# Performance work log

Measured on AMD Instinct MI355X. Metric: run time of the kernel, lower is better.

The kernel has to match this reference:

```python
import jax, jax.numpy as jnp
import numpy as np


def _conv2d(x, w, stride, padding):
    # x: NCHW, w: OIHW
    return jax.lax.conv_general_dilated(
        x, w, window_strides=(stride, stride),
        padding=((padding, padding), (padding, padding)),
        dimension_numbers=('NCHW', 'OIHW', 'NCHW'))


def setup_inputs() -> dict:
    key = jax.random.key(0)
    k1, k2 = jax.random.split(key)
    B, C_in, H, Wd = 8, 64, 256, 256
    C_out, ksz = 64, 3
    x = jax.random.normal(k1, (B, C_in, H, Wd), dtype=jnp.float32)
    W = jax.random.normal(k2, (C_out, C_in, ksz, ksz), dtype=jnp.float32)
    b = jnp.zeros((C_out,), dtype=jnp.float32)
    return {"x": x, "W": W, "b": b}


def reference(x, W, b):
    stride, padding = 1, 1
    B, C, H, Wd = x.shape
    # per-pixel (across-channel) normalization of activations
    xf = jnp.transpose(x, (0, 2, 3, 1)).reshape(-1, C)       # [B*H*W, C]
    mu = jnp.mean(xf, axis=-1, keepdims=True)
    var = jnp.mean((xf - mu) ** 2, axis=-1, keepdims=True)    # unbiased=False
    r = 1.0 / jnp.sqrt(var + 1e-8)
    y_norm = r * (xf - mu)
    # int8 fake-quant per pixel
    s_act = 127.0 / jnp.maximum(jnp.max(jnp.abs(y_norm), axis=-1, keepdims=True), 1e-8)
    y_tilde = jnp.clip(jnp.round(s_act * y_norm), -128.0, 127.0) / s_act
    y4 = jnp.transpose(y_tilde.reshape(B, H, Wd, C), (0, 3, 1, 2))
    # ternary weight quant (value; STE only matters for backward)
    s_w = 1.0 / jnp.maximum(jnp.mean(jnp.abs(W)), 1e-8)
    w_tilde = jnp.clip(jnp.round(s_w * W), -1.0, 1.0) / s_w
    out = _conv2d(y4, w_tilde, stride, padding) + b[None, :, None, None]
    return out
```

## Files before the change

kernel.cpp:

```cpp
#include <hip/hip_runtime.h>

typedef _Float16 half8 __attribute__((ext_vector_type(8)));
typedef float    f32x4 __attribute__((ext_vector_type(4)));

#define NB   8
#define NC   64
#define NH   256
#define NW   256
#define NO   64
#define HT   4
#define TW_OFF   0ull
#define TW_BYTES (576ull * 64ull * 2ull)
#define MSW_OFF  (TW_OFF + TW_BYTES)
#define PART_OFF (MSW_OFF + 16ull)

__global__ __launch_bounds__(256) void wsum_kernel(const float* __restrict__ W,
                                                   float* __restrict__ partial) {
    __shared__ float red[256];
    int tid = threadIdx.x;
    red[tid] = fabsf(W[blockIdx.x * 256 + tid]);
    __syncthreads();
    for (int off = 128; off > 0; off >>= 1) {
        if (tid < off) red[tid] += red[tid + off];
        __syncthreads();
    }
    if (tid == 0) partial[blockIdx.x] = red[0];
}

__global__ __launch_bounds__(256) void wq2_kernel(const float* __restrict__ W,
                                                  const float* __restrict__ partial,
                                                  _Float16* __restrict__ tw2,
                                                  float* __restrict__ msw_out) {
    __shared__ float red[256];
    int tid = threadIdx.x;
    red[tid] = (tid < 144) ? partial[tid] : 0.0f;
    __syncthreads();
    for (int off = 128; off > 0; off >>= 1) {
        if (tid < off) red[tid] += red[tid + off];
        __syncthreads();
    }
    float mean = red[0] / 36864.0f;
    float msw  = fmaxf(mean, 1e-8f);
    float s_w  = 1.0f / msw;
    if (blockIdx.x == 0 && tid == 0) msw_out[0] = msw;

    int idx = blockIdx.x * 256 + tid;
    float t = rintf(s_w * W[idx]);
    t = fminf(1.0f, fmaxf(-1.0f, t));
    int o  = idx / 576;
    int r  = idx - o * 576;
    int c  = r / 9;
    int r2 = r - c * 9;
    int kh = r2 / 3;
    int kw = r2 - kh * 3;
    int k  = (kh * 3 + kw) * 64 + c;
    tw2[((k >> 3) * 64 + o) * 8 + (k & 7)] = (_Float16)t;
}

__global__ __launch_bounds__(256, 3) void fused_kernel(const float* __restrict__ x,
                                                       const _Float16* __restrict__ tw2,
                                                       const float* __restrict__ msw_p,
                                                       const float* __restrict__ bias,
                                                       float* __restrict__ out) {
    __shared__ alignas(16) _Float16 lds[6 * 8 * 66 * 8];

    int tid = threadIdx.x;
    int pb  = blockIdx.x;
    int bid = (pb & 7) * 256 + (pb >> 3);
    int wt = bid & 3;
    int ht = (bid >> 2) & 63;
    int bb = bid >> 8;
    int h0 = ht * HT;
    int w0 = wt * 64;

    for (int p = tid; p < 396; p += 256) {
        int kh = p / 66;
        int wl = p - kh * 66;
        int hp = h0 + kh - 1;
        int wp = w0 + wl - 1;
        _Float16* slot = lds + kh * 4224 + wl * 8;

        if (((unsigned)hp >= 256u) | ((unsigned)wp >= 256u)) {
            half8 z;
            #pragma unroll
            for (int j = 0; j < 8; ++j) z[j] = (_Float16)0.0f;
            #pragma unroll
            for (int cc = 0; cc < 8; ++cc) *(half8*)(slot + cc * 528) = z;
            continue;
        }
        const float* xp = x + (size_t)bb * 4194304 + (size_t)hp * 256 + wp;

        float s = 0.0f, sq = 0.0f, mn = 1e30f, mx = -1e30f;
        #pragma unroll
        for (int cc = 0; cc < 8; ++cc) {
            half8 hv;
            #pragma unroll
            for (int j = 0; j < 8; ++j) {
                float v = xp[(size_t)(cc * 8 + j) * 65536];
                s  += v;
                sq += v * v;
                mn = fminf(mn, v);
                mx = fmaxf(mx, v);
                hv[j] = (_Float16)v;
            }
            *(half8*)(slot + cc * 528) = hv;
        }
        float mu  = s * (1.0f / 64.0f);
        float var = fmaxf(sq * (1.0f / 64.0f) - mu * mu, 0.0f);
        float r    = 1.0f / sqrtf(var + 1e-8f);
        float dmax = fmaxf(mx - mu, mu - mn);
        float amax = fmaxf(dmax * r, 1e-8f);
        float s_a  = 127.0f / amax;
        float invs = amax / 127.0f;
        float af   = s_a * r;
        float bf   = -mu * af;

        #pragma unroll
        for (int cc = 0; cc < 8; ++cc) {
            half8 hv = *(half8*)(slot + cc * 528);
            #pragma unroll
            for (int j = 0; j < 8; ++j) {
                float q = rintf(fmaf((float)hv[j], af, bf));
                q = fminf(127.0f, fmaxf(-128.0f, q));
                hv[j] = (_Float16)(q * invs);
            }
            *(half8*)(slot + cc * 528) = hv;
        }
    }

    int l   = tid & 63;
    int wv  = tid >> 6;
    int l15 = l & 15;
    int q8  = l >> 4;

    half8 aw[18];
    #pragma unroll
    for (int ks = 0; ks < 18; ++ks)
        aw[ks] = *(const half8*)(tw2 + (((ks * 4 + q8) * 64) + wv * 16 + l15) * 8);

    __syncthreads();

    float msw = *msw_p;
    #pragma unroll
    for (int r = 0; r < HT; ++r) {
        f32x4 acc[4];
        #pragma unroll
        for (int nt = 0; nt < 4; ++nt)
            #pragma unroll
            for (int r2 = 0; r2 < 4; ++r2) acc[nt][r2] = 0.0f;

        #pragma unroll
        for (int ks = 0; ks < 18; ++ks) {
            int tap = ks >> 1;
            int kh  = tap / 3;
            int kw  = tap - kh * 3;
            int ccb = (ks & 1) * 4 + q8;
            int base = (((kh + r) * 8 + ccb) * 66 + kw + l15) * 8;
            #pragma unroll
            for (int nt = 0; nt < 4; ++nt) {
                half8 bf = *(const half8*)(lds + base + nt * 128);
                acc[nt] = __builtin_amdgcn_mfma_f32_16x16x32_f16(aw[ks], bf, acc[nt], 0, 0, 0);
            }
        }

        size_t obase = ((size_t)bb * 64) * 65536 + (size_t)(h0 + r) * 256;
        #pragma unroll
        for (int reg = 0; reg < 4; ++reg) {
            int o = wv * 16 + q8 * 4 + reg;
            float bo = bias[o];
            #pragma unroll
            for (int nt = 0; nt < 4; ++nt) {
                int w = w0 + nt * 16 + l15;
                out[obase + (size_t)o * 65536 + w] = acc[nt][reg] * msw + bo;
            }
        }
    }
}

extern "C" void kernel_launch(void* const* d_in, const int* in_sizes, int n_in,
                              void* d_out, int out_size, void* d_ws, size_t ws_size,
                              hipStream_t stream) {
    const float* x = (const float*)d_in[0];
    const float* W = (const float*)d_in[1];
    const float* b = (const float*)d_in[2];
    float* out = (float*)d_out;

    char* ws = (char*)d_ws;
    _Float16* tw2  = (_Float16*)(ws + TW_OFF);
    float*    msw  = (float*)(ws + MSW_OFF);
    float*    part = (float*)(ws + PART_OFF);

    wsum_kernel<<<144, 256, 0, stream>>>(W, part);
    wq2_kernel<<<144, 256, 0, stream>>>(W, part, tw2, msw);
    fused_kernel<<<2048, 256, 0, stream>>>(x, tw2, msw, b, out);
}
```

Baseline: 285.0 us.

## Retile MFMA work per wave to 2x2 output-channel by column tiles

Each wave now computes a 32-output-channel by 32-column tile rather than 16 channels by 64 columns. This halves the LDS B-fragment reads per MFMA, at the cost of twice as many weight registers (36 half8). The weight loads are hoisted ahead of the normalization loop so they overlap it, and occupancy is lowered from 3 to 2 blocks per CU. The int8 clamp is also removed, on the reasoning that the rounded value cannot exceed the range by construction.

```diff
diff --git a/kernel.cpp b/kernel.cpp
--- a/kernel.cpp
+++ b/kernel.cpp
@@ -57,7 +57,7 @@
     tw2[((k >> 3) * 64 + o) * 8 + (k & 7)] = (_Float16)t;
 }
 
-__global__ __launch_bounds__(256, 3) void fused_kernel(const float* __restrict__ x,
+__global__ __launch_bounds__(256, 2) void fused_kernel(const float* __restrict__ x,
                                                        const _Float16* __restrict__ tw2,
                                                        const float* __restrict__ msw_p,
                                                        const float* __restrict__ bias,
@@ -72,6 +72,22 @@
     int bb = bid >> 8;
     int h0 = ht * HT;
     int w0 = wt * 64;
+
+    int l   = tid & 63;
+    int wv  = tid >> 6;
+    int l15 = l & 15;
+    int q8  = l >> 4;
+    int ogp = wv >> 1;
+    int ntp = wv & 1;
+
+    half8 aw[36];
+    #pragma unroll
+    for (int ks = 0; ks < 18; ++ks) {
+        #pragma unroll
+        for (int i = 0; i < 2; ++i)
+            aw[ks * 2 + i] =
+                *(const half8*)(tw2 + (((ks * 4 + q8) * 64) + ogp * 32 + i * 16 + l15) * 8);
+    }
 
     for (int p = tid; p < 396; p += 256) {
         int kh = p / 66;
@@ -121,33 +137,24 @@
             #pragma unroll
             for (int j = 0; j < 8; ++j) {
                 float q = rintf(fmaf((float)hv[j], af, bf));
-                q = fminf(127.0f, fmaxf(-128.0f, q));
                 hv[j] = (_Float16)(q * invs);
             }
             *(half8*)(slot + cc * 528) = hv;
         }
     }
 
-    int l   = tid & 63;
-    int wv  = tid >> 6;
-    int l15 = l & 15;
-    int q8  = l >> 4;
-
-    half8 aw[18];
-    #pragma unroll
-    for (int ks = 0; ks < 18; ++ks)
-        aw[ks] = *(const half8*)(tw2 + (((ks * 4 + q8) * 64) + wv * 16 + l15) * 8);
-
     __syncthreads();
 
     float msw = *msw_p;
     #pragma unroll
     for (int r = 0; r < HT; ++r) {
-        f32x4 acc[4];
-        #pragma unroll
-        for (int nt = 0; nt < 4; ++nt)
-            #pragma unroll
-            for (int r2 = 0; r2 < 4; ++r2) acc[nt][r2] = 0.0f;
+        f32x4 acc[2][2];
+        #pragma unroll
+        for (int i = 0; i < 2; ++i)
+            #pragma unroll
+            for (int j = 0; j < 2; ++j)
+                #pragma unroll
+                for (int r2 = 0; r2 < 4; ++r2) acc[i][j][r2] = 0.0f;
 
         #pragma unroll
         for (int ks = 0; ks < 18; ++ks) {
@@ -156,22 +163,26 @@
             int kw  = tap - kh * 3;
             int ccb = (ks & 1) * 4 + q8;
             int base = (((kh + r) * 8 + ccb) * 66 + kw + l15) * 8;
-            #pragma unroll
-            for (int nt = 0; nt < 4; ++nt) {
-                half8 bf = *(const half8*)(lds + base + nt * 128);
-                acc[nt] = __builtin_amdgcn_mfma_f32_16x16x32_f16(aw[ks], bf, acc[nt], 0, 0, 0);
-            }
+            half8 b0 = *(const half8*)(lds + base + (ntp * 2 + 0) * 128);
+            half8 b1 = *(const half8*)(lds + base + (ntp * 2 + 1) * 128);
+            acc[0][0] = __builtin_amdgcn_mfma_f32_16x16x32_f16(aw[ks * 2 + 0], b0, acc[0][0], 0, 0, 0);
+            acc[1][0] = __builtin_amdgcn_mfma_f32_16x16x32_f16(aw[ks * 2 + 1], b0, acc[1][0], 0, 0, 0);
+            acc[0][1] = __builtin_amdgcn_mfma_f32_16x16x32_f16(aw[ks * 2 + 0], b1, acc[0][1], 0, 0, 0);
+            acc[1][1] = __builtin_amdgcn_mfma_f32_16x16x32_f16(aw[ks * 2 + 1], b1, acc[1][1], 0, 0, 0);
         }
 
         size_t obase = ((size_t)bb * 64) * 65536 + (size_t)(h0 + r) * 256;
         #pragma unroll
-        for (int reg = 0; reg < 4; ++reg) {
-            int o = wv * 16 + q8 * 4 + reg;
-            float bo = bias[o];
-            #pragma unroll
-            for (int nt = 0; nt < 4; ++nt) {
-                int w = w0 + nt * 16 + l15;
-                out[obase + (size_t)o * 65536 + w] = acc[nt][reg] * msw + bo;
+        for (int i = 0; i < 2; ++i) {
+            #pragma unroll
+            for (int reg = 0; reg < 4; ++reg) {
+                int o = ogp * 32 + i * 16 + q8 * 4 + reg;
+                float bo = bias[o];
+                #pragma unroll
+                for (int j = 0; j < 2; ++j) {
+                    int w = w0 + (ntp * 2 + j) * 16 + l15;
+                    out[obase + (size_t)o * 65536 + w] = acc[i][j][reg] * msw + bo;
+                }
             }
         }
     }
```

Measured after the change: 277.6 us. 2.6% less time.
